# Kernel tuning notes

Hardware: AMD Instinct MI355X
Metric: run time of the kernel (lower is better)

Reference implementation:

```python
import jax, jax.numpy as jnp
import numpy as np

N_NODES = 100000
N_EDGES = 1600000
DIM = 128
N_FILTERS = 64
N_GAUSS = 50
CUTOFF = 5.0


def setup_inputs() -> dict:
    key = jax.random.key(0)
    ks = jax.random.split(key, 10)
    x = jax.random.normal(ks[0], (N_NODES, DIM), dtype=jnp.float32)
    edge_index = jax.random.randint(ks[1], (2, N_EDGES), 0, N_NODES, dtype=jnp.int64)
    dist = jax.random.uniform(ks[2], (N_EDGES,), dtype=jnp.float32) * CUTOFF
    edge_weight = dist
    edge_attr = dist
    # CFConv params
    lin1_w = jax.random.normal(ks[3], (N_FILTERS, DIM), dtype=jnp.float32) * 0.05   # no bias
    lin2_w = jax.random.normal(ks[4], (DIM, N_FILTERS), dtype=jnp.float32) * 0.05
    lin2_b = jnp.zeros((DIM,), dtype=jnp.float32)
    # edge_nn: Linear(50->64), ReLU, Linear(64->64)
    enn1_w = jax.random.normal(ks[5], (N_FILTERS, N_GAUSS), dtype=jnp.float32) * 0.1
    enn1_b = jnp.zeros((N_FILTERS,), dtype=jnp.float32)
    enn2_w = jax.random.normal(ks[6], (N_FILTERS, N_FILTERS), dtype=jnp.float32) * 0.1
    enn2_b = jnp.zeros((N_FILTERS,), dtype=jnp.float32)
    return {"x": x, "edge_index": edge_index, "edge_weight": edge_weight,
            "edge_attr": edge_attr, "lin1_w": lin1_w, "lin2_w": lin2_w,
            "lin2_b": lin2_b, "enn1_w": enn1_w, "enn1_b": enn1_b,
            "enn2_w": enn2_w, "enn2_b": enn2_b}


def reference(x, edge_index, edge_weight, edge_attr,
              lin1_w, lin2_w, lin2_b, enn1_w, enn1_b, enn2_w, enn2_b):
    n_nodes = x.shape[0]
    # GaussianSmearing(0, cutoff, 50)
    offset = jnp.linspace(0.0, CUTOFF, N_GAUSS).astype(jnp.float32)
    coeff = -0.5 / (offset[1] - offset[0]) ** 2
    smeared = jnp.exp(coeff * (edge_attr[:, None] - offset[None, :]) ** 2)  # [E, 50]
    # edge filter MLP + cosine cutoff (PyG CFConv)
    h_edge = jax.nn.relu(smeared @ enn1_w.T + enn1_b)
    W = h_edge @ enn2_w.T + enn2_b                                         # [E, 64]
    C = 0.5 * (jnp.cos(edge_weight * jnp.pi / CUTOFF) + 1.0)
    W = W * C[:, None]
    # gather -> multiply -> scatter-add (aggr='add', flow source_to_target)
    h = x @ lin1_w.T                                                       # [N, 64]
    src, dst = edge_index[0], edge_index[1]
    msg = h[src] * W                                                       # [E, 64]
    agg = jax.ops.segment_sum(msg, dst, num_segments=n_nodes)              # [N, 64]
    y = agg @ lin2_w.T + lin2_b                                            # [N, 128]
    # activation (relu), dropout p=0 (identity), residual
    y = jax.nn.relu(y)
    return x + y
```

## Files before the change

kernel.cpp:

```cpp
#include <hip/hip_runtime.h>
#include <hip/hip_bf16.h>

#define NNODES 100000
#define NEDGES 1600000
#define DIM    128
#define NF     64
#define NG     50
#define EPG    52
#define EPW    208
#define NWAVES 8192
#define EPTOT  1703936

#define BSH    9
#define NBKT   ((NNODES + 511) >> 9)
#define CHK    8192
#define NCHK   ((NEDGES + CHK - 1) / CHK)

#define NBIN   16385

constexpr float F_CUTOFF = 5.0f;
constexpr float F_DELTA  = F_CUTOFF / (NG - 1);
constexpr float F_COEFF  = -0.5f / (F_DELTA * F_DELTA);
constexpr float F_PI     = 3.14159265358979323846f;
constexpr float TSCALE   = 16384.0f / F_CUTOFF;

typedef __attribute__((ext_vector_type(8))) short short8v;
typedef __attribute__((ext_vector_type(4))) float f32x4;

__device__ inline unsigned short f2bf(float x) {
  __hip_bfloat16 h = __float2bfloat16(x);
  return *reinterpret_cast<unsigned short*>(&h);
}
__device__ inline unsigned pkbf(float a, float b) {
  float2 f2; f2.x = a; f2.y = b;
  __hip_bfloat162 h2 = __float22bfloat162_rn(f2);
  return *reinterpret_cast<unsigned*>(&h2);
}
__device__ inline float bf2f(unsigned int lo16) {
  return __uint_as_float(lo16 << 16);
}

__global__ __launch_bounds__(256, 2) void k_lin1_mfma(
    const float* __restrict__ x, const float* __restrict__ w1,
    unsigned short* __restrict__ h) {
  const int wave = threadIdx.x >> 6, lane = threadIdx.x & 63;
  const int lo = lane & 15, g = lane >> 4;

  short8v B[4][4];
#pragma unroll
  for (int t = 0; t < 4; ++t) {
    const int j = (t >> 1) * 32 + 2 * lo + (t & 1);
#pragma unroll
    for (int s = 0; s < 4; ++s) {
      union { short8v v; unsigned u[4]; } bu;
      const float* wr = w1 + j * DIM + s * 32 + g * 8;
#pragma unroll
      for (int p = 0; p < 4; ++p)
        bu.u[p] = pkbf(wr[2 * p], wr[2 * p + 1]);
      B[t][s] = bu.v;
    }
  }

  const int nIter = NNODES / 16;
  for (int it = blockIdx.x * 4 + wave; it < nIter; it += gridDim.x * 4) {
    const int n0 = it * 16;
    short8v A[4];
#pragma unroll
    for (int s = 0; s < 4; ++s) {
      const float4 va = *(const float4*)&x[(size_t)(n0 + lo) * DIM + s * 32 + g * 8];
      const float4 vb = *(const float4*)&x[(size_t)(n0 + lo) * DIM + s * 32 + g * 8 + 4];
      union { short8v v; unsigned u[4]; } au;
      au.u[0] = pkbf(va.x, va.y);
      au.u[1] = pkbf(va.z, va.w);
      au.u[2] = pkbf(vb.x, vb.y);
      au.u[3] = pkbf(vb.z, vb.w);
      A[s] = au.v;
    }
    f32x4 acc[4];
#pragma unroll
    for (int t = 0; t < 4; ++t) {
      f32x4 z = {0.f, 0.f, 0.f, 0.f};
      z = __builtin_amdgcn_mfma_f32_16x16x32_bf16(A[0], B[t][0], z, 0, 0, 0);
      z = __builtin_amdgcn_mfma_f32_16x16x32_bf16(A[1], B[t][1], z, 0, 0, 0);
      z = __builtin_amdgcn_mfma_f32_16x16x32_bf16(A[2], B[t][2], z, 0, 0, 0);
      z = __builtin_amdgcn_mfma_f32_16x16x32_bf16(A[3], B[t][3], z, 0, 0, 0);
      acc[t] = z;
    }
#pragma unroll
    for (int r = 0; r < 4; ++r) {
      unsigned short* hp = h + (size_t)(n0 + g * 4 + r) * NF + 2 * lo;
      *(unsigned*)(hp)      = pkbf(acc[0][r], acc[1][r]);
      *(unsigned*)(hp + 32) = pkbf(acc[2][r], acc[3][r]);
    }
  }
}

__global__ __launch_bounds__(256) void k_table(
    const float* __restrict__ w1, const float* __restrict__ b1,
    const float* __restrict__ w2, const float* __restrict__ b2,
    unsigned short* __restrict__ tab) {
  __shared__ float ssm[4][56];
  __shared__ float sh1[4][64];
  const int wave = threadIdx.x >> 6, lane = threadIdx.x & 63;
  const int wid = blockIdx.x * 4 + wave;
  const float b1v = b1[lane], b2v = b2[lane];
  for (int bin = wid; bin < NBIN; bin += 1024) {
    const float d = (float)bin * (F_CUTOFF / 16384.0f);
    if (lane < NG) {
      const float t0 = d - (float)lane * F_DELTA;
      ssm[wave][lane] = __expf(F_COEFF * t0 * t0);
    }
    float h1 = b1v;
#pragma unroll
    for (int gg = 0; gg < NG; ++gg)
      h1 = fmaf(ssm[wave][gg], w1[lane * NG + gg], h1);
    sh1[wave][lane] = fmaxf(h1, 0.f);
    float wv = b2v;
#pragma unroll
    for (int f = 0; f < NF; ++f)
      wv = fmaf(sh1[wave][f], w2[lane * NF + f], wv);
    const float C = 0.5f * (__cosf(d * (F_PI / F_CUTOFF)) + 1.0f);
    tab[(size_t)bin * NF + lane] = f2bf(wv * C);
  }
}

__global__ __launch_bounds__(1024) void k_bhist(
    const int* __restrict__ ei, int* __restrict__ gcnt) {
  __shared__ int lcnt[NBKT];
  for (int i = threadIdx.x; i < NBKT; i += 1024) lcnt[i] = 0;
  __syncthreads();
  const int base = blockIdx.x * CHK;
  for (int i = threadIdx.x; i < CHK; i += 1024) {
    const int e = base + i;
    if (e < NEDGES) atomicAdd(&lcnt[ei[NEDGES + e] >> BSH], 1);
  }
  __syncthreads();
  for (int i = threadIdx.x; i < NBKT; i += 1024)
    if (lcnt[i]) atomicAdd(&gcnt[i], lcnt[i]);
}

__global__ __launch_bounds__(256) void k_bscan(
    const int* __restrict__ gcnt, int* __restrict__ boff, int* __restrict__ bcur) {
  __shared__ int sb[256];
  const int t = threadIdx.x;
  const int v = (t < NBKT) ? gcnt[t] : 0;
  sb[t] = v;
  __syncthreads();
  for (int off = 1; off < 256; off <<= 1) {
    const int xv = (t >= off) ? sb[t - off] : 0;
    __syncthreads();
    sb[t] += xv;
    __syncthreads();
  }
  if (t <= NBKT) {
    const int ex = sb[t] - v;
    boff[t] = ex;
    if (t < NBKT) bcur[t] = ex;
  }
}

__global__ __launch_bounds__(1024) void k_bscatter(
    const int* __restrict__ ei, const float* __restrict__ ea,
    int* __restrict__ bcur, int2* __restrict__ sd8S, int* __restrict__ sdstS) {
  __shared__ int lcnt[NBKT];
  __shared__ int lcur[NBKT];
  for (int i = threadIdx.x; i < NBKT; i += 1024) lcnt[i] = 0;
  __syncthreads();
  const int base = blockIdx.x * CHK;
  for (int i = threadIdx.x; i < CHK; i += 1024) {
    const int e = base + i;
    if (e < NEDGES) atomicAdd(&lcnt[ei[NEDGES + e] >> BSH], 1);
  }
  __syncthreads();
  for (int i = threadIdx.x; i < NBKT; i += 1024)
    lcur[i] = lcnt[i] ? atomicAdd(&bcur[i], lcnt[i]) : 0;
  __syncthreads();
  for (int i = threadIdx.x; i < CHK; i += 1024) {
    const int e = base + i;
    if (e < NEDGES) {
      const int dst = ei[NEDGES + e];
      const int pos = atomicAdd(&lcur[dst >> BSH], 1);
      int2 r; r.x = ei[e]; r.y = __float_as_int(ea[e]);
      sd8S[pos]  = r;
      sdstS[pos] = dst;
    }
  }
}

__global__ __launch_bounds__(1024) void k_bsort(
    const int2* __restrict__ sd8S, const int* __restrict__ sdstS,
    const int* __restrict__ boff, int4* __restrict__ srec) {
  __shared__ int cnt[512];
  __shared__ int red[512];
  const int b = blockIdx.x;
  const int t = threadIdx.x;
  const int s0 = boff[b], s1 = boff[b + 1];
  const int nodeBase = b << BSH;
  if (t < 512) cnt[t] = 0;
  __syncthreads();
  for (int i = s0 + t; i < s1; i += 1024)
    atomicAdd(&cnt[sdstS[i] - nodeBase], 1);
  __syncthreads();
  const int v = (t < 512) ? cnt[t] : 0;
  if (t < 512) red[t] = v;
  __syncthreads();
  for (int off = 1; off < 512; off <<= 1) {
    int xv = 0;
    if (t < 512 && t >= off) xv = red[t - off];
    __syncthreads();
    if (t < 512) red[t] += xv;
    __syncthreads();
  }
  if (t < 512) cnt[t] = s0 + red[t] - v;
  __syncthreads();
  for (int i = s0 + t; i < s1; i += 1024) {
    const int2 r8 = sd8S[i];
    const int dst = sdstS[i];
    const int p = atomicAdd(&cnt[dst - nodeBase], 1);
    int4 r; r.x = r8.x; r.y = r8.y; r.z = dst; r.w = 0;
    srec[p] = r;
  }
}

__global__ __launch_bounds__(256) void k_edge_tab(
    const int4* __restrict__ srec, const unsigned short* __restrict__ hbf,
    const unsigned* __restrict__ tab, unsigned short* __restrict__ agg) {
  const int wave = threadIdx.x >> 6, lane = threadIdx.x & 63;
  const int lo = lane & 15, g = lane >> 4;

  const int wid   = blockIdx.x * 4 + wave;
  const int gbase = wid * EPW + g * EPG;

  int run_dst = -1;
  float c0 = 0.f, c1 = 0.f, c2 = 0.f, c3 = 0.f;

  int4 q0 = srec[gbase + 0];
  int4 q1 = srec[gbase + 1];
  int4 q2 = srec[gbase + 2];
  int4 q3 = srec[gbase + 3];

#pragma unroll 1
  for (int it = 0; it < EPG / 4; ++it) {
    const int eg = gbase + it * 4;
    const int4 r0 = q0, r1 = q1, r2 = q2, r3 = q3;
    {
      const int itn = (it + 1 < EPG / 4) ? it + 1 : it;
      const int egn = gbase + itn * 4;
      q0 = srec[egn + 0]; q1 = srec[egn + 1];
      q2 = srec[egn + 2]; q3 = srec[egn + 3];
    }

    int   sv[4] = {r0.x, r1.x, r2.x, r3.x};
    float dd[4] = {__int_as_float(r0.y), __int_as_float(r1.y),
                   __int_as_float(r2.y), __int_as_float(r3.y)};
    int   dv[4] = {r0.z, r1.z, r2.z, r3.z};
#pragma unroll
    for (int r = 0; r < 4; ++r) {
      const bool val = (eg + r) < NEDGES;
      sv[r] = val ? sv[r] : 0;
      dv[r] = val ? dv[r] : -1;
    }

    unsigned hp0[4], hp1[4];
#pragma unroll
    for (int r = 0; r < 4; ++r) {
      const unsigned short* hs = hbf + (size_t)sv[r] * NF + 2 * lo;
      hp0[r] = *(const unsigned*)(hs);
      hp1[r] = *(const unsigned*)(hs + 32);
    }

    unsigned tw0[4], tw1[4];
#pragma unroll
    for (int r = 0; r < 4; ++r) {
      const float dcl = fminf(fmaxf(dd[r], 0.f), F_CUTOFF);
      int bn = (int)(dcl * TSCALE + 0.5f);
      bn = (bn > 16384) ? 16384 : bn;
      const unsigned* trow = tab + (size_t)bn * (NF / 2);
      tw0[r] = trow[lo];
      tw1[r] = trow[16 + lo];
    }

#pragma unroll
    for (int r = 0; r < 4; ++r) {
      const float m0 = bf2f(hp0[r] & 0xffffu) * bf2f(tw0[r] & 0xffffu);
      const float m1 = bf2f(hp0[r] >> 16)     * bf2f(tw0[r] >> 16);
      const float m2 = bf2f(hp1[r] & 0xffffu) * bf2f(tw1[r] & 0xffffu);
      const float m3 = bf2f(hp1[r] >> 16)     * bf2f(tw1[r] >> 16);
      if (dv[r] != run_dst) {
        if (run_dst >= 0) {
          unsigned short* ap = agg + (size_t)run_dst * NF + 2 * lo;
          const unsigned k0 = pkbf(c0, c1), k1 = pkbf(c2, c3);
          asm volatile("global_atomic_pk_add_bf16 %0, %1, off" :: "v"(ap), "v"(k0));
          asm volatile("global_atomic_pk_add_bf16 %0, %1, off" :: "v"(ap + 32), "v"(k1));
        }
        c0 = 0.f; c1 = 0.f; c2 = 0.f; c3 = 0.f;
        run_dst = dv[r];
      }
      c0 += m0; c1 += m1; c2 += m2; c3 += m3;
    }
  }
  if (run_dst >= 0) {
    unsigned short* ap = agg + (size_t)run_dst * NF + 2 * lo;
    const unsigned k0 = pkbf(c0, c1), k1 = pkbf(c2, c3);
    asm volatile("global_atomic_pk_add_bf16 %0, %1, off" :: "v"(ap), "v"(k0));
    asm volatile("global_atomic_pk_add_bf16 %0, %1, off" :: "v"(ap + 32), "v"(k1));
  }
}

__global__ __launch_bounds__(256) void k_out(
    const float* __restrict__ x, const unsigned short* __restrict__ agg,
    const float* __restrict__ w2, const float* __restrict__ b,
    float* __restrict__ out) {
  __shared__ __align__(16) float sw[DIM][NF + 4];
  __shared__ __align__(16) float sa[4][4][NF];
  for (int i = threadIdx.x; i < DIM * NF; i += 256)
    sw[i >> 6][i & 63] = w2[i];
  __syncthreads();
  const int wave = threadIdx.x >> 6, lane = threadIdx.x & 63;
  const float bias0 = b[lane], bias1 = b[lane + 64];
  const int nIter = NNODES / 4;
  for (int it = blockIdx.x * 4 + wave; it < nIter; it += gridDim.x * 4) {
    const int n0 = it * 4;
#pragma unroll
    for (int i = 0; i < 4; ++i)
      sa[wave][i][lane] = bf2f((unsigned)agg[(size_t)(n0 + i) * NF + lane]);
    float acc[8];
#pragma unroll
    for (int i = 0; i < 4; ++i) { acc[2 * i] = bias0; acc[2 * i + 1] = bias1; }
#pragma unroll
    for (int j4 = 0; j4 < NF / 4; ++j4) {
      const float4 wv0 = *(const float4*)&sw[lane][j4 * 4];
      const float4 wv1 = *(const float4*)&sw[lane + 64][j4 * 4];
#pragma unroll
      for (int i = 0; i < 4; ++i) {
        const float4 av = *(const float4*)&sa[wave][i][j4 * 4];
        acc[2 * i]     = fmaf(wv0.x, av.x, acc[2 * i]);
        acc[2 * i]     = fmaf(wv0.y, av.y, acc[2 * i]);
        acc[2 * i]     = fmaf(wv0.z, av.z, acc[2 * i]);
        acc[2 * i]     = fmaf(wv0.w, av.w, acc[2 * i]);
        acc[2 * i + 1] = fmaf(wv1.x, av.x, acc[2 * i + 1]);
        acc[2 * i + 1] = fmaf(wv1.y, av.y, acc[2 * i + 1]);
        acc[2 * i + 1] = fmaf(wv1.z, av.z, acc[2 * i + 1]);
        acc[2 * i + 1] = fmaf(wv1.w, av.w, acc[2 * i + 1]);
      }
    }
#pragma unroll
    for (int i = 0; i < 4; ++i) {
      const size_t base = (size_t)(n0 + i) * DIM;
      out[base + lane]      = x[base + lane]      + fmaxf(acc[2 * i],     0.f);
      out[base + 64 + lane] = x[base + 64 + lane] + fmaxf(acc[2 * i + 1], 0.f);
    }
  }
}

extern "C" void kernel_launch(void* const* d_in, const int* in_sizes, int n_in,
                              void* d_out, int out_size, void* d_ws, size_t ws_size,
                              hipStream_t stream) {
  const float* x   = (const float*)d_in[0];
  const int*   ei  = (const int*)  d_in[1];
  const float* ea  = (const float*)d_in[3];
  const float* l1w = (const float*)d_in[4];
  const float* l2w = (const float*)d_in[5];
  const float* l2b = (const float*)d_in[6];
  const float* e1w = (const float*)d_in[7];
  const float* e1b = (const float*)d_in[8];
  const float* e2w = (const float*)d_in[9];
  const float* e2b = (const float*)d_in[10];
  float* out = (float*)d_out;

  char* p = (char*)d_ws;
  unsigned short* hbf = (unsigned short*)p; p += (size_t)NNODES * NF * 2;
  unsigned short* agg = (unsigned short*)p; p += (size_t)NNODES * NF * 2;
  int2* sd8S  = (int2*)p;                   p += (size_t)NEDGES * 8;
  int*  sdstS = (int*)p;                    p += (size_t)NEDGES * 4;
  unsigned short* tab = (unsigned short*)p; p += (size_t)16512 * NF * 2;
  int*  gcnt  = (int*)p;                    p += 1024 * 4;
  int*  boff  = (int*)p;                    p += 1024 * 4;
  int*  bcur  = (int*)p;                    p += 1024 * 4;

  int4* srec = (int4*)d_out;

  hipMemsetAsync(gcnt, 0, 1024 * sizeof(int), stream);
  hipMemsetAsync(agg, 0, sizeof(unsigned short) * (size_t)NNODES * NF, stream);

  k_table   <<<256, 256, 0, stream>>>(e1w, e1b, e2w, e2b, tab);
  k_lin1_mfma<<<512, 256, 0, stream>>>(x, l1w, hbf);
  k_bhist   <<<NCHK, 1024, 0, stream>>>(ei, gcnt);
  k_bscan   <<<1, 256, 0, stream>>>(gcnt, boff, bcur);
  k_bscatter<<<NCHK, 1024, 0, stream>>>(ei, ea, bcur, sd8S, sdstS);
  k_bsort   <<<NBKT, 1024, 0, stream>>>(sd8S, sdstS, boff, srec);
  k_edge_tab<<<NWAVES / 4, 256, 0, stream>>>((const int4*)srec, hbf, (const unsigned*)tab, agg);
  k_out     <<<2048, 256, 0, stream>>>(x, agg, l2w, l2b, out);
}
```

Baseline: 168.8 us.

## Fuse front kernels, pack edge records to 8 bytes, precompute table bins

Merges the lin1 MFMA, bucket histogram and filter-table kernels into one launch, with block ranges assigning the roles. Edge records shrink from 16 to 8 bytes by packing the source index (17 bits) and the table bin index into one word next to dst. The bin is computed during scatter, and the separate dst array is removed. The scatter keeps edge data in registers across both passes instead of re-reading it, and the edge kernel gets an XCD-style block swizzle. This cuts global traffic through the sort and edge stages and saves launches, but relies on node ids fitting in 17 bits.

```diff
diff --git a/kernel.cpp b/kernel.cpp
--- a/kernel.cpp
+++ b/kernel.cpp
@@ -18,6 +18,12 @@
 
 #define NBIN   16385
 
+#define LIN1_BLOCKS 512
+#define BH_CHK      2048
+#define BH_BLOCKS   ((NEDGES + BH_CHK - 1) / BH_CHK)
+#define TAB_BLOCKS  64
+#define FRONT_BLOCKS (LIN1_BLOCKS + BH_BLOCKS + TAB_BLOCKS)
+
 constexpr float F_CUTOFF = 5.0f;
 constexpr float F_DELTA  = F_CUTOFF / (NG - 1);
 constexpr float F_COEFF  = -0.5f / (F_DELTA * F_DELTA);
@@ -40,103 +46,100 @@
   return __uint_as_float(lo16 << 16);
 }
 
-__global__ __launch_bounds__(256, 2) void k_lin1_mfma(
-    const float* __restrict__ x, const float* __restrict__ w1,
-    unsigned short* __restrict__ h) {
+__global__ __launch_bounds__(256) void k_front(
+    const float* __restrict__ x, const float* __restrict__ l1w,
+    unsigned short* __restrict__ hbf,
+    const int* __restrict__ ei, int* __restrict__ gcnt,
+    const float* __restrict__ e1w, const float* __restrict__ e1b,
+    const float* __restrict__ e2w, const float* __restrict__ e2b,
+    unsigned short* __restrict__ tab) {
+  const int bid  = blockIdx.x;
   const int wave = threadIdx.x >> 6, lane = threadIdx.x & 63;
-  const int lo = lane & 15, g = lane >> 4;
-
-  short8v B[4][4];
-#pragma unroll
-  for (int t = 0; t < 4; ++t) {
-    const int j = (t >> 1) * 32 + 2 * lo + (t & 1);
-#pragma unroll
-    for (int s = 0; s < 4; ++s) {
-      union { short8v v; unsigned u[4]; } bu;
-      const float* wr = w1 + j * DIM + s * 32 + g * 8;
-#pragma unroll
-      for (int p = 0; p < 4; ++p)
-        bu.u[p] = pkbf(wr[2 * p], wr[2 * p + 1]);
-      B[t][s] = bu.v;
-    }
-  }
-
-  const int nIter = NNODES / 16;
-  for (int it = blockIdx.x * 4 + wave; it < nIter; it += gridDim.x * 4) {
-    const int n0 = it * 16;
-    short8v A[4];
-#pragma unroll
-    for (int s = 0; s < 4; ++s) {
-      const float4 va = *(const float4*)&x[(size_t)(n0 + lo) * DIM + s * 32 + g * 8];
-      const float4 vb = *(const float4*)&x[(size_t)(n0 + lo) * DIM + s * 32 + g * 8 + 4];
-      union { short8v v; unsigned u[4]; } au;
-      au.u[0] = pkbf(va.x, va.y);
-      au.u[1] = pkbf(va.z, va.w);
-      au.u[2] = pkbf(vb.x, vb.y);
-      au.u[3] = pkbf(vb.z, vb.w);
-      A[s] = au.v;
-    }
-    f32x4 acc[4];
+
+  if (bid < LIN1_BLOCKS) {
+    const int lo = lane & 15, g = lane >> 4;
+    short8v B[4][4];
 #pragma unroll
     for (int t = 0; t < 4; ++t) {
-      f32x4 z = {0.f, 0.f, 0.f, 0.f};
-      z = __builtin_amdgcn_mfma_f32_16x16x32_bf16(A[0], B[t][0], z, 0, 0, 0);
-      z = __builtin_amdgcn_mfma_f32_16x16x32_bf16(A[1], B[t][1], z, 0, 0, 0);
-      z = __builtin_amdgcn_mfma_f32_16x16x32_bf16(A[2], B[t][2], z, 0, 0, 0);
-      z = __builtin_amdgcn_mfma_f32_16x16x32_bf16(A[3], B[t][3], z, 0, 0, 0);
-      acc[t] = z;
-    }
-#pragma unroll
-    for (int r = 0; r < 4; ++r) {
-      unsigned short* hp = h + (size_t)(n0 + g * 4 + r) * NF + 2 * lo;
-      *(unsigned*)(hp)      = pkbf(acc[0][r], acc[1][r]);
-      *(unsigned*)(hp + 32) = pkbf(acc[2][r], acc[3][r]);
-    }
-  }
-}
-
-__global__ __launch_bounds__(256) void k_table(
-    const float* __restrict__ w1, const float* __restrict__ b1,
-    const float* __restrict__ w2, const float* __restrict__ b2,
-    unsigned short* __restrict__ tab) {
-  __shared__ float ssm[4][56];
-  __shared__ float sh1[4][64];
-  const int wave = threadIdx.x >> 6, lane = threadIdx.x & 63;
-  const int wid = blockIdx.x * 4 + wave;
-  const float b1v = b1[lane], b2v = b2[lane];
-  for (int bin = wid; bin < NBIN; bin += 1024) {
-    const float d = (float)bin * (F_CUTOFF / 16384.0f);
-    if (lane < NG) {
-      const float t0 = d - (float)lane * F_DELTA;
-      ssm[wave][lane] = __expf(F_COEFF * t0 * t0);
-    }
-    float h1 = b1v;
-#pragma unroll
-    for (int gg = 0; gg < NG; ++gg)
-      h1 = fmaf(ssm[wave][gg], w1[lane * NG + gg], h1);
-    sh1[wave][lane] = fmaxf(h1, 0.f);
-    float wv = b2v;
-#pragma unroll
-    for (int f = 0; f < NF; ++f)
-      wv = fmaf(sh1[wave][f], w2[lane * NF + f], wv);
-    const float C = 0.5f * (__cosf(d * (F_PI / F_CUTOFF)) + 1.0f);
-    tab[(size_t)bin * NF + lane] = f2bf(wv * C);
-  }
-}
-
-__global__ __launch_bounds__(1024) void k_bhist(
-    const int* __restrict__ ei, int* __restrict__ gcnt) {
-  __shared__ int lcnt[NBKT];
-  for (int i = threadIdx.x; i < NBKT; i += 1024) lcnt[i] = 0;
-  __syncthreads();
-  const int base = blockIdx.x * CHK;
-  for (int i = threadIdx.x; i < CHK; i += 1024) {
-    const int e = base + i;
-    if (e < NEDGES) atomicAdd(&lcnt[ei[NEDGES + e] >> BSH], 1);
-  }
-  __syncthreads();
-  for (int i = threadIdx.x; i < NBKT; i += 1024)
-    if (lcnt[i]) atomicAdd(&gcnt[i], lcnt[i]);
+      const int j = (t >> 1) * 32 + 2 * lo + (t & 1);
+#pragma unroll
+      for (int s = 0; s < 4; ++s) {
+        union { short8v v; unsigned u[4]; } bu;
+        const float* wr = l1w + j * DIM + s * 32 + g * 8;
+#pragma unroll
+        for (int p = 0; p < 4; ++p)
+          bu.u[p] = pkbf(wr[2 * p], wr[2 * p + 1]);
+        B[t][s] = bu.v;
+      }
+    }
+    const int nIter = NNODES / 16;
+    for (int it = bid * 4 + wave; it < nIter; it += LIN1_BLOCKS * 4) {
+      const int n0 = it * 16;
+      short8v A[4];
+#pragma unroll
+      for (int s = 0; s < 4; ++s) {
+        const float4 va = *(const float4*)&x[(size_t)(n0 + lo) * DIM + s * 32 + g * 8];
+        const float4 vb = *(const float4*)&x[(size_t)(n0 + lo) * DIM + s * 32 + g * 8 + 4];
+        union { short8v v; unsigned u[4]; } au;
+        au.u[0] = pkbf(va.x, va.y);
+        au.u[1] = pkbf(va.z, va.w);
+        au.u[2] = pkbf(vb.x, vb.y);
+        au.u[3] = pkbf(vb.z, vb.w);
+        A[s] = au.v;
+      }
+      f32x4 acc[4];
+#pragma unroll
+      for (int t = 0; t < 4; ++t) {
+        f32x4 z = {0.f, 0.f, 0.f, 0.f};
+        z = __builtin_amdgcn_mfma_f32_16x16x32_bf16(A[0], B[t][0], z, 0, 0, 0);
+        z = __builtin_amdgcn_mfma_f32_16x16x32_bf16(A[1], B[t][1], z, 0, 0, 0);
+        z = __builtin_amdgcn_mfma_f32_16x16x32_bf16(A[2], B[t][2], z, 0, 0, 0);
+        z = __builtin_amdgcn_mfma_f32_16x16x32_bf16(A[3], B[t][3], z, 0, 0, 0);
+        acc[t] = z;
+      }
+#pragma unroll
+      for (int r = 0; r < 4; ++r) {
+        unsigned short* hp = hbf + (size_t)(n0 + g * 4 + r) * NF + 2 * lo;
+        *(unsigned*)(hp)      = pkbf(acc[0][r], acc[1][r]);
+        *(unsigned*)(hp + 32) = pkbf(acc[2][r], acc[3][r]);
+      }
+    }
+  } else if (bid < LIN1_BLOCKS + BH_BLOCKS) {
+    __shared__ int lcnt[NBKT];
+    for (int i = threadIdx.x; i < NBKT; i += 256) lcnt[i] = 0;
+    __syncthreads();
+    const int base = (bid - LIN1_BLOCKS) * BH_CHK;
+    for (int i = threadIdx.x; i < BH_CHK; i += 256) {
+      const int e = base + i;
+      if (e < NEDGES) atomicAdd(&lcnt[ei[NEDGES + e] >> BSH], 1);
+    }
+    __syncthreads();
+    for (int i = threadIdx.x; i < NBKT; i += 256)
+      if (lcnt[i]) atomicAdd(&gcnt[i], lcnt[i]);
+  } else {
+    __shared__ float ssm[4][56];
+    __shared__ float sh1[4][64];
+    const int wid = (bid - LIN1_BLOCKS - BH_BLOCKS) * 4 + wave;
+    const float b1v = e1b[lane], b2v = e2b[lane];
+    for (int bin = wid; bin < NBIN; bin += TAB_BLOCKS * 4) {
+      const float d = (float)bin * (F_CUTOFF / 16384.0f);
+      if (lane < NG) {
+        const float t0 = d - (float)lane * F_DELTA;
+        ssm[wave][lane] = __expf(F_COEFF * t0 * t0);
+      }
+      float h1 = b1v;
+#pragma unroll
+      for (int gg = 0; gg < NG; ++gg)
+        h1 = fmaf(ssm[wave][gg], e1w[lane * NG + gg], h1);
+      sh1[wave][lane] = fmaxf(h1, 0.f);
+      float wv = b2v;
+#pragma unroll
+      for (int f = 0; f < NF; ++f)
+        wv = fmaf(sh1[wave][f], e2w[lane * NF + f], wv);
+      const float C = 0.5f * (__cosf(d * (F_PI / F_CUTOFF)) + 1.0f);
+      tab[(size_t)bin * NF + lane] = f2bf(wv * C);
+    }
+  }
 }
 
 __global__ __launch_bounds__(256) void k_bscan(
@@ -161,35 +164,43 @@
 
 __global__ __launch_bounds__(1024) void k_bscatter(
     const int* __restrict__ ei, const float* __restrict__ ea,
-    int* __restrict__ bcur, int2* __restrict__ sd8S, int* __restrict__ sdstS) {
+    int* __restrict__ bcur, int2* __restrict__ spack) {
   __shared__ int lcnt[NBKT];
   __shared__ int lcur[NBKT];
-  for (int i = threadIdx.x; i < NBKT; i += 1024) lcnt[i] = 0;
+  const int t = threadIdx.x;
+  for (int i = t; i < NBKT; i += 1024) lcnt[i] = 0;
   __syncthreads();
   const int base = blockIdx.x * CHK;
-  for (int i = threadIdx.x; i < CHK; i += 1024) {
-    const int e = base + i;
-    if (e < NEDGES) atomicAdd(&lcnt[ei[NEDGES + e] >> BSH], 1);
-  }
-  __syncthreads();
-  for (int i = threadIdx.x; i < NBKT; i += 1024)
+  int dsts[8], srcs[8]; float eav[8];
+#pragma unroll
+  for (int k = 0; k < 8; ++k) {
+    const int e = base + t + k * 1024;
+    const bool v = e < NEDGES;
+    dsts[k] = v ? ei[NEDGES + e] : -1;
+    srcs[k] = v ? ei[e] : 0;
+    eav[k]  = v ? ea[e] : 0.f;
+    if (v) atomicAdd(&lcnt[dsts[k] >> BSH], 1);
+  }
+  __syncthreads();
+  for (int i = t; i < NBKT; i += 1024)
     lcur[i] = lcnt[i] ? atomicAdd(&bcur[i], lcnt[i]) : 0;
   __syncthreads();
-  for (int i = threadIdx.x; i < CHK; i += 1024) {
-    const int e = base + i;
-    if (e < NEDGES) {
-      const int dst = ei[NEDGES + e];
-      const int pos = atomicAdd(&lcur[dst >> BSH], 1);
-      int2 r; r.x = ei[e]; r.y = __float_as_int(ea[e]);
-      sd8S[pos]  = r;
-      sdstS[pos] = dst;
+#pragma unroll
+  for (int k = 0; k < 8; ++k) {
+    if (dsts[k] >= 0) {
+      const int pos = atomicAdd(&lcur[dsts[k] >> BSH], 1);
+      const float dcl = fminf(fmaxf(eav[k], 0.f), F_CUTOFF);
+      int bn = (int)(dcl * TSCALE + 0.5f);
+      bn = (bn > 16384) ? 16384 : bn;
+      int2 r; r.x = srcs[k] | (bn << 17); r.y = dsts[k];
+      spack[pos] = r;
     }
   }
 }
 
 __global__ __launch_bounds__(1024) void k_bsort(
-    const int2* __restrict__ sd8S, const int* __restrict__ sdstS,
-    const int* __restrict__ boff, int4* __restrict__ srec) {
+    const int2* __restrict__ spack, const int* __restrict__ boff,
+    int2* __restrict__ srec) {
   __shared__ int cnt[512];
   __shared__ int red[512];
   const int b = blockIdx.x;
@@ -199,7 +210,7 @@
   if (t < 512) cnt[t] = 0;
   __syncthreads();
   for (int i = s0 + t; i < s1; i += 1024)
-    atomicAdd(&cnt[sdstS[i] - nodeBase], 1);
+    atomicAdd(&cnt[spack[i].y - nodeBase], 1);
   __syncthreads();
   const int v = (t < 512) ? cnt[t] : 0;
   if (t < 512) red[t] = v;
@@ -214,51 +225,50 @@
   if (t < 512) cnt[t] = s0 + red[t] - v;
   __syncthreads();
   for (int i = s0 + t; i < s1; i += 1024) {
-    const int2 r8 = sd8S[i];
-    const int dst = sdstS[i];
-    const int p = atomicAdd(&cnt[dst - nodeBase], 1);
-    int4 r; r.x = r8.x; r.y = r8.y; r.z = dst; r.w = 0;
+    const int2 r = spack[i];
+    const int p = atomicAdd(&cnt[r.y - nodeBase], 1);
     srec[p] = r;
   }
 }
 
 __global__ __launch_bounds__(256) void k_edge_tab(
-    const int4* __restrict__ srec, const unsigned short* __restrict__ hbf,
+    const int2* __restrict__ srec, const unsigned short* __restrict__ hbf,
     const unsigned* __restrict__ tab, unsigned short* __restrict__ agg) {
   const int wave = threadIdx.x >> 6, lane = threadIdx.x & 63;
   const int lo = lane & 15, g = lane >> 4;
 
-  const int wid   = blockIdx.x * 4 + wave;
+  const int bid = blockIdx.x;
+  const int bsw = (bid & 7) * 256 + (bid >> 3);
+  const int wid = bsw * 4 + wave;
   const int gbase = wid * EPW + g * EPG;
 
   int run_dst = -1;
   float c0 = 0.f, c1 = 0.f, c2 = 0.f, c3 = 0.f;
 
-  int4 q0 = srec[gbase + 0];
-  int4 q1 = srec[gbase + 1];
-  int4 q2 = srec[gbase + 2];
-  int4 q3 = srec[gbase + 3];
+  const int4* sp4 = (const int4*)srec;
+  int4 qa = sp4[gbase / 2];
+  int4 qb = sp4[gbase / 2 + 1];
 
 #pragma unroll 1
   for (int it = 0; it < EPG / 4; ++it) {
     const int eg = gbase + it * 4;
-    const int4 r0 = q0, r1 = q1, r2 = q2, r3 = q3;
+    const int4 ca = qa, cb = qb;
     {
       const int itn = (it + 1 < EPG / 4) ? it + 1 : it;
       const int egn = gbase + itn * 4;
-      q0 = srec[egn + 0]; q1 = srec[egn + 1];
-      q2 = srec[egn + 2]; q3 = srec[egn + 3];
-    }
-
-    int   sv[4] = {r0.x, r1.x, r2.x, r3.x};
-    float dd[4] = {__int_as_float(r0.y), __int_as_float(r1.y),
-                   __int_as_float(r2.y), __int_as_float(r3.y)};
-    int   dv[4] = {r0.z, r1.z, r2.z, r3.z};
+      qa = sp4[egn / 2];
+      qb = sp4[egn / 2 + 1];
+    }
+
+    const int px[4] = {ca.x, ca.z, cb.x, cb.z};
+    const int py[4] = {ca.y, ca.w, cb.y, cb.w};
+    int sv[4], dv[4], bnv[4];
 #pragma unroll
     for (int r = 0; r < 4; ++r) {
       const bool val = (eg + r) < NEDGES;
-      sv[r] = val ? sv[r] : 0;
-      dv[r] = val ? dv[r] : -1;
+      sv[r]  = val ? (px[r] & 0x1FFFF) : 0;
+      bnv[r] = val ? ((unsigned)px[r] >> 17) : 0;
+      dv[r]  = val ? py[r] : -1;
     }
 
     unsigned hp0[4], hp1[4];
@@ -268,14 +278,10 @@
       hp0[r] = *(const unsigned*)(hs);
       hp1[r] = *(const unsigned*)(hs + 32);
     }
-
     unsigned tw0[4], tw1[4];
 #pragma unroll
     for (int r = 0; r < 4; ++r) {
-      const float dcl = fminf(fmaxf(dd[r], 0.f), F_CUTOFF);
-      int bn = (int)(dcl * TSCALE + 0.5f);
-      bn = (bn > 16384) ? 16384 : bn;
-      const unsigned* trow = tab + (size_t)bn * (NF / 2);
+      const unsigned* trow = tab + (size_t)bnv[r] * (NF / 2);
       tw0[r] = trow[lo];
       tw1[r] = trow[16 + lo];
     }
@@ -371,24 +377,22 @@
   char* p = (char*)d_ws;
   unsigned short* hbf = (unsigned short*)p; p += (size_t)NNODES * NF * 2;
   unsigned short* agg = (unsigned short*)p; p += (size_t)NNODES * NF * 2;
-  int2* sd8S  = (int2*)p;                   p += (size_t)NEDGES * 8;
-  int*  sdstS = (int*)p;                    p += (size_t)NEDGES * 4;
+  int2* spack = (int2*)p;                   p += (size_t)NEDGES * 8;
   unsigned short* tab = (unsigned short*)p; p += (size_t)16512 * NF * 2;
   int*  gcnt  = (int*)p;                    p += 1024 * 4;
   int*  boff  = (int*)p;                    p += 1024 * 4;
   int*  bcur  = (int*)p;                    p += 1024 * 4;
 
-  int4* srec = (int4*)d_out;
+  int2* srec = (int2*)d_out;
 
   hipMemsetAsync(gcnt, 0, 1024 * sizeof(int), stream);
   hipMemsetAsync(agg, 0, sizeof(unsigned short) * (size_t)NNODES * NF, stream);
 
-  k_table   <<<256, 256, 0, stream>>>(e1w, e1b, e2w, e2b, tab);
-  k_lin1_mfma<<<512, 256, 0, stream>>>(x, l1w, hbf);
-  k_bhist   <<<NCHK, 1024, 0, stream>>>(ei, gcnt);
+  k_front   <<<FRONT_BLOCKS, 256, 0, stream>>>(x, l1w, hbf, ei, gcnt,
+                                               e1w, e1b, e2w, e2b, tab);
   k_bscan   <<<1, 256, 0, stream>>>(gcnt, boff, bcur);
-  k_bscatter<<<NCHK, 1024, 0, stream>>>(ei, ea, bcur, sd8S, sdstS);
-  k_bsort   <<<NBKT, 1024, 0, stream>>>(sd8S, sdstS, boff, srec);
-  k_edge_tab<<<NWAVES / 4, 256, 0, stream>>>((const int4*)srec, hbf, (const unsigned*)tab, agg);
+  k_bscatter<<<NCHK, 1024, 0, stream>>>(ei, ea, bcur, spack);
+  k_bsort   <<<NBKT, 1024, 0, stream>>>(spack, boff, srec);
+  k_edge_tab<<<2048, 256, 0, stream>>>(srec, hbf, (const unsigned*)tab, agg);
   k_out     <<<2048, 256, 0, stream>>>(x, agg, l2w, l2b, out);
 }
```

Result: slower. 188.5 us (+11.7%).
